# Kernel tuning notes

Measured on AMD Instinct MI355X. Metric: run time of the kernel, lower is better.

## Reference

```python
import jax, jax.numpy as jnp
import numpy as np

B, L, H, N = 4, 4096, 1024, 16
EPS = 1e-6  # layer_norm_epsilon


def setup_inputs() -> dict:
    key = jax.random.key(0)
    ks = jax.random.split(key, 8)
    hidden_states = jax.random.normal(ks[0], (B, L, H), dtype=jnp.float32)
    attention_mask = jnp.ones((B, L), dtype=jnp.float32)
    norm_weight = jnp.ones((H,), dtype=jnp.float32)
    # S4D init: dt log-uniform in [1e-3, 1e-1]; S4D-Lin A init; random C, D
    dt_min, dt_max = 1e-3, 1e-1
    log_dt = jax.random.uniform(ks[1], (H,), dtype=jnp.float32) * (
        float(np.log(dt_max)) - float(np.log(dt_min))) + float(np.log(dt_min))
    log_A_real = jnp.log(0.5 * jnp.ones((H, N), dtype=jnp.float32))
    A_imag = jnp.broadcast_to(float(np.pi) * jnp.arange(N, dtype=jnp.float32), (H, N))
    C_real = jax.random.normal(ks[2], (H, N), dtype=jnp.float32) * (0.5 ** 0.5)
    C_imag = jax.random.normal(ks[3], (H, N), dtype=jnp.float32) * (0.5 ** 0.5)
    D = jax.random.normal(ks[4], (H,), dtype=jnp.float32)
    out_w = jax.random.normal(ks[5], (2 * H, H), dtype=jnp.float32) * 0.02  # 1x1 conv to 2H (GLU)
    out_b = jnp.zeros((2 * H,), dtype=jnp.float32)
    return dict(hidden_states=hidden_states, attention_mask=attention_mask,
                norm_weight=norm_weight, log_dt=log_dt, log_A_real=log_A_real,
                A_imag=A_imag, C_real=C_real, C_imag=C_imag, D=D,
                out_w=out_w, out_b=out_b)


def _s4d_kernel(log_dt, log_A_real, A_imag, C_real, C_imag, length):
    """Diagonal SSM convolution kernel k[h, l] (S4D ZOH discretization)."""
    dt = jnp.exp(log_dt)                                   # (H,)
    A = -jnp.exp(log_A_real) + 1j * A_imag                 # (H, N) complex64
    C = C_real + 1j * C_imag                               # (H, N)
    dtA = A * dt[:, None]                                  # (H, N)
    C_disc = C * (jnp.exp(dtA) - 1.0) / A                  # (H, N)
    vand = jnp.exp(dtA[:, :, None] * jnp.arange(length, dtype=jnp.float32))  # (H, N, L)
    k = 2.0 * jnp.einsum('hn,hnl->hl', C_disc, vand).real  # (H, L)
    return k.astype(jnp.float32)


def reference(hidden_states, attention_mask, norm_weight, log_dt, log_A_real,
              A_imag, C_real, C_imag, D, out_w, out_b):
    # LongT5LayerNorm: RMSNorm (no mean subtraction), variance in fp32
    var = jnp.mean(jnp.square(hidden_states.astype(jnp.float32)), axis=-1, keepdims=True)
    normed = hidden_states * jax.lax.rsqrt(var + EPS) * norm_weight  # (B, L, H)
    # mask padded positions, go to channel-major layout (B, H, L)
    u = (normed * attention_mask[..., None]).transpose(0, 2, 1)
    Lx = u.shape[-1]
    k = _s4d_kernel(log_dt, log_A_real, A_imag, C_real, C_imag, Lx)  # (H, L)
    # causal convolution via FFT of length 2L
    nfft = 2 * Lx
    k_f = jnp.fft.rfft(k, n=nfft)                 # (H, nfft//2+1)
    u_f = jnp.fft.rfft(u, n=nfft)                 # (B, H, nfft//2+1)
    y = jnp.fft.irfft(u_f * k_f, n=nfft)[..., :Lx]  # (B, H, L)
    y = y + u * D[:, None]                        # skip connection
    y = jax.nn.gelu(y, approximate=False)         # torch nn.GELU (exact)
    # output 1x1 conv to 2H, then GLU over the channel dim
    z = jnp.einsum('bhl,oh->bol', y, out_w) + out_b[:, None]
    a, b = jnp.split(z, 2, axis=1)
    ssm_out = (a * jax.nn.sigmoid(b)).transpose(0, 2, 1)  # (B, L, H)
    # residual + dropout (eval mode -> identity)
    return hidden_states + ssm_out
```

## Files before the change

### kernel.cpp

```cpp
#include <hip/hip_runtime.h>

#define B_   4
#define L_   4096
#define H_   1024
#define N_   16
#define CH_  64
#define NC_  (L_/CH_)
#define M_   (B_*L_)
#define O2_  (2*H_)
#define EPS_ 1e-6f

typedef __attribute__((ext_vector_type(4))) float  f32x4;
typedef __attribute__((ext_vector_type(8))) __bf16 bf16x8;

__device__ __forceinline__ unsigned short f2bf(float x) {
  union { float f; unsigned int u; } v; v.f = x;
  unsigned int r = v.u + 0x7FFFu + ((v.u >> 16) & 1u);
  return (unsigned short)(r >> 16);
}
__device__ __forceinline__ float bf2f(unsigned short x) {
  union { unsigned int u; float f; } v; v.u = ((unsigned int)x) << 16;
  return v.f;
}

__device__ __forceinline__ void async_copy16(const void* g, void* l) {
  __builtin_amdgcn_global_load_lds(
      (const __attribute__((address_space(1))) unsigned int*)g,
      (__attribute__((address_space(3))) unsigned int*)l, 16, 0, 0);
}

__global__ void k_prep(const float* __restrict__ log_dt,
                       const float* __restrict__ log_A_real,
                       const float* __restrict__ A_imag,
                       const float* __restrict__ C_real,
                       const float* __restrict__ C_imag,
                       const float* __restrict__ outw,
                       const float* __restrict__ outb,
                       float* __restrict__ wr,  float* __restrict__ wi,
                       float* __restrict__ c2r, float* __restrict__ c2i,
                       float* __restrict__ wpr, float* __restrict__ wpi,
                       unsigned short* __restrict__ Wbf,
                       float* __restrict__ bp) {
  int idx = blockIdx.x * 256 + threadIdx.x;
  int p = idx >> 10, hh = idx & (H_ - 1);
  size_t src = (size_t)((p >> 1) + (p & 1) * H_) * H_ + hh;
  Wbf[idx] = f2bf(outw[src]);
  if (idx < O2_) bp[idx] = outb[(idx >> 1) + (idx & 1) * H_];
  if (idx < H_ * N_) {
    int h = idx / N_, n = idx % N_;
    int hn = h * N_ + n;
    float dt  = expf(log_dt[h]);
    float Ar  = -expf(log_A_real[hn]);
    float Ai  = A_imag[hn];
    float dr  = Ar * dt, di = Ai * dt;
    float er  = expf(dr);
    float wrv = er * cosf(di), wiv = er * sinf(di);
    float e1r = wrv - 1.0f, e1i = wiv;
    float den = Ar * Ar + Ai * Ai;
    float qr  = (e1r * Ar + e1i * Ai) / den;
    float qi  = (e1i * Ar - e1r * Ai) / den;
    float Cr  = C_real[hn], Ci = C_imag[hn];
    float cdr = Cr * qr - Ci * qi;
    float cdi = Cr * qi + Ci * qr;
    float ep  = expf((float)CH_ * dr);
    int o = n * H_ + h;
    wr[o]  = wrv;  wi[o]  = wiv;
    c2r[o] = 2.0f * cdr; c2i[o] = 2.0f * cdi;
    wpr[o] = ep * cosf((float)CH_ * di);
    wpi[o] = ep * sinf((float)CH_ * di);
  }
}

__global__ __launch_bounds__(256) void k_scale(const float* __restrict__ hs,
                                               const float* __restrict__ mask,
                                               float* __restrict__ scale) {
  int m = blockIdx.x, tid = threadIdx.x;
  float4 v = reinterpret_cast<const float4*>(hs + (size_t)m * H_)[tid];
  float s = v.x * v.x + v.y * v.y + v.z * v.z + v.w * v.w;
  #pragma unroll
  for (int off = 32; off > 0; off >>= 1) s += __shfl_down(s, off, 64);
  __shared__ float ps[4];
  if ((tid & 63) == 0) ps[tid >> 6] = s;
  __syncthreads();
  if (tid == 0) {
    float var = (ps[0] + ps[1] + ps[2] + ps[3]) * (1.0f / H_);
    scale[m] = rsqrtf(var + EPS_) * mask[m];
  }
}

__global__ __launch_bounds__(256) void k_scan1(const float* __restrict__ hs,
                                               const float* __restrict__ nw,
                                               const float* __restrict__ scale,
                                               const float* __restrict__ wr_,
                                               const float* __restrict__ wi_,
                                               float* __restrict__ endr,
                                               float* __restrict__ endi,
                                               unsigned short* __restrict__ ubf) {
  int tid = threadIdx.x;
  int h = blockIdx.x * 256 + tid;
  int c = blockIdx.y, b = blockIdx.z;
  float wr[N_], wi[N_], xr[N_], xi[N_];
  #pragma unroll
  for (int n = 0; n < N_; n++) {
    wr[n] = wr_[n * H_ + h]; wi[n] = wi_[n * H_ + h];
    xr[n] = 0.f; xi[n] = 0.f;
  }
  float nwh = nw[h];
  __shared__ float ssc[CH_];
  int l0 = c * CH_;
  if (tid < CH_) ssc[tid] = scale[(size_t)b * L_ + l0 + tid];
  __syncthreads();
  const float* hp = hs + ((size_t)b * L_ + l0) * H_ + h;
  unsigned short* up = ubf + ((size_t)b * L_ + l0) * H_ + h;
  #pragma unroll 8
  for (int l = 0; l < CH_; l++) {
    float u = hp[(size_t)l * H_] * ssc[l] * nwh;
    unsigned short ub = f2bf(u);
    up[(size_t)l * H_] = ub;
    u = bf2f(ub);
    #pragma unroll
    for (int n = 0; n < N_; n++) {
      float oxr = xr[n];
      xr[n] = fmaf(wr[n], oxr, fmaf(-wi[n], xi[n], u));
      xi[n] = fmaf(wr[n], xi[n], wi[n] * oxr);
    }
  }
  size_t base = (((size_t)b * NC_ + c) * N_) * H_ + h;
  #pragma unroll
  for (int n = 0; n < N_; n++) {
    endr[base + (size_t)n * H_] = xr[n];
    endi[base + (size_t)n * H_] = xi[n];
  }
}

__global__ __launch_bounds__(256) void k_carry(const float* __restrict__ wpr_,
                                               const float* __restrict__ wpi_,
                                               const float* __restrict__ endr,
                                               const float* __restrict__ endi,
                                               float* __restrict__ carr,
                                               float* __restrict__ cari) {
  int idx = blockIdx.x * 256 + threadIdx.x;
  int h = idx & (H_ - 1);
  int n = (idx >> 10) & (N_ - 1);
  int b = idx >> 14;
  float wprv = wpr_[n * H_ + h], wpiv = wpi_[n * H_ + h];
  float sr = 0.f, si = 0.f;
  size_t cstride = (size_t)N_ * H_;
  size_t base = ((size_t)b * NC_) * cstride + (size_t)n * H_ + h;
  for (int c = 0; c < NC_; c++, base += cstride) {
    carr[base] = sr; cari[base] = si;
    float er = endr[base], ei = endi[base];
    float osr = sr;
    sr = fmaf(wprv, osr,  fmaf(-wpiv, si, er));
    si = fmaf(wprv, si, fmaf(wpiv, osr, ei));
  }
}

__global__ __launch_bounds__(256) void k_scan2(const unsigned short* __restrict__ ubf,
                                               const float* __restrict__ wr_,
                                               const float* __restrict__ wi_,
                                               const float* __restrict__ c2r_,
                                               const float* __restrict__ c2i_,
                                               const float* __restrict__ Dp,
                                               const float* __restrict__ carr,
                                               const float* __restrict__ cari,
                                               unsigned short* __restrict__ ybf) {
  int tid = threadIdx.x;
  int h = blockIdx.x * 256 + tid;
  int c = blockIdx.y, b = blockIdx.z;
  float wr[N_], wi[N_], cr[N_], ci[N_], xr[N_], xi[N_];
  size_t base = (((size_t)b * NC_ + c) * N_) * H_ + h;
  #pragma unroll
  for (int n = 0; n < N_; n++) {
    wr[n] = wr_[n * H_ + h]; wi[n] = wi_[n * H_ + h];
    cr[n] = c2r_[n * H_ + h]; ci[n] = c2i_[n * H_ + h];
    xr[n] = carr[base + (size_t)n * H_];
    xi[n] = cari[base + (size_t)n * H_];
  }
  float Dh = Dp[h];
  int l0 = c * CH_;
  const unsigned short* up = ubf + ((size_t)b * L_ + l0) * H_ + h;
  unsigned short* yp = ybf + ((size_t)b * L_ + l0) * H_ + h;
  #pragma unroll 8
  for (int l = 0; l < CH_; l++) {
    float u = bf2f(up[(size_t)l * H_]);
    float yv = u * Dh;
    #pragma unroll
    for (int n = 0; n < N_; n++) {
      float oxr = xr[n];
      xr[n] = fmaf(wr[n], oxr, fmaf(-wi[n], xi[n], u));
      xi[n] = fmaf(wr[n], xi[n], wi[n] * oxr);
      yv = fmaf(cr[n], xr[n], yv);
      yv = fmaf(-ci[n], xi[n], yv);
    }
    float g = 0.5f * yv * (1.0f + erff(yv * 0.70710678118654752f));
    yp[(size_t)l * H_] = f2bf(g);
  }
}

#define BM 128
#define BN 128
#define BK 32
#define GSTRIDE 68
__global__ __launch_bounds__(256) void k_gemm(const unsigned short* __restrict__ A,
                                              const unsigned short* __restrict__ Bw,
                                              const float* __restrict__ bp,
                                              const float* __restrict__ hs,
                                              float* __restrict__ out) {
  __shared__ __align__(16) char smem[BM * GSTRIDE * 4];
  unsigned short* As = (unsigned short*)smem;
  unsigned short* Bs = As + BM * BK;
  float* gt = (float*)smem;
  const int tid  = threadIdx.x;
  const int lane = tid & 63;
  const int wave = tid >> 6;
  const int bn = blockIdx.x * BN;
  const int bm = blockIdx.y * BM;
  const int wm = (wave >> 1) * 64;
  const int wn = (wave & 1) * 64;
  const int K = H_;
  f32x4 acc[4][4];
  #pragma unroll
  for (int mi = 0; mi < 4; mi++)
    #pragma unroll
    for (int ni = 0; ni < 4; ni++) acc[mi][ni] = (f32x4){0.f, 0.f, 0.f, 0.f};

  const int g0 = tid, g1 = 256 + tid;
  const int r0 = g0 >> 2, c0 = ((g0 & 3) ^ ((r0 >> 1) & 3)) * 8;
  const int r1 = g1 >> 2, c1 = ((g1 & 3) ^ ((r1 >> 1) & 3)) * 8;
  const int ar = lane & 15, kqi = lane >> 4;

  for (int k0 = 0; k0 < K; k0 += BK) {
    async_copy16(A  + (size_t)(bm + r0) * K + k0 + c0, &As[g0 * 8]);
    async_copy16(A  + (size_t)(bm + r1) * K + k0 + c1, &As[g1 * 8]);
    async_copy16(Bw + (size_t)(bn + r0) * K + k0 + c0, &Bs[g0 * 8]);
    async_copy16(Bw + (size_t)(bn + r1) * K + k0 + c1, &Bs[g1 * 8]);
    __syncthreads();
    bf16x8 af[4], bf[4];
    #pragma unroll
    for (int mi = 0; mi < 4; mi++) {
      int row = wm + mi * 16 + ar;
      af[mi] = *reinterpret_cast<const bf16x8*>(&As[row * BK + ((kqi ^ ((row >> 1) & 3)) * 8)]);
    }
    #pragma unroll
    for (int ni = 0; ni < 4; ni++) {
      int row = wn + ni * 16 + ar;
      bf[ni] = *reinterpret_cast<const bf16x8*>(&Bs[row * BK + ((kqi ^ ((row >> 1) & 3)) * 8)]);
    }
    #pragma unroll
    for (int mi = 0; mi < 4; mi++)
      #pragma unroll
      for (int ni = 0; ni < 4; ni++)
        acc[mi][ni] = __builtin_amdgcn_mfma_f32_16x16x32_bf16(af[mi], bf[ni], acc[mi][ni], 0, 0, 0);
    __syncthreads();
  }
  #pragma unroll
  for (int ni = 0; ni < 4; ni++) {
    int p  = wn + ni * 16 + (lane & 15);
    int pe = (bn + p) & ~1;
    float bA = bp[pe], bB = bp[pe + 1];
    int jl = p >> 1;
    #pragma unroll
    for (int mi = 0; mi < 4; mi++) {
      int row0 = wm + mi * 16 + (lane >> 4) * 4;
      #pragma unroll
      for (int r = 0; r < 4; r++) {
        float v = acc[mi][ni][r];
        float w = __shfl_xor(v, 1, 64);
        if (!(lane & 1))
          gt[(row0 + r) * GSTRIDE + jl] = (v + bA) / (1.0f + __expf(-(w + bB)));
      }
    }
  }
  __syncthreads();
  {
    int c4 = tid & 15;
    int rr = tid >> 4;
    size_t obase = (size_t)bm * H_ + (bn >> 1);
    #pragma unroll
    for (int rep = 0; rep < 8; rep++) {
      int row = rep * 16 + rr;
      float4 g = *reinterpret_cast<const float4*>(&gt[row * GSTRIDE + c4 * 4]);
      size_t o = obase + (size_t)row * H_ + c4 * 4;
      float4 hv = *reinterpret_cast<const float4*>(&hs[o]);
      float4 rv = {hv.x + g.x, hv.y + g.y, hv.z + g.z, hv.w + g.w};
      *reinterpret_cast<float4*>(&out[o]) = rv;
    }
  }
}

extern "C" void kernel_launch(void* const* d_in, const int* in_sizes, int n_in,
                              void* d_out, int out_size, void* d_ws, size_t ws_size,
                              hipStream_t stream) {
  const float* hs    = (const float*)d_in[0];
  const float* mask  = (const float*)d_in[1];
  const float* nw    = (const float*)d_in[2];
  const float* ldt   = (const float*)d_in[3];
  const float* lar   = (const float*)d_in[4];
  const float* aim   = (const float*)d_in[5];
  const float* crl   = (const float*)d_in[6];
  const float* cim   = (const float*)d_in[7];
  const float* Dp    = (const float*)d_in[8];
  const float* outw  = (const float*)d_in[9];
  const float* outb  = (const float*)d_in[10];
  float* out = (float*)d_out;

  size_t off = 0;
  char* ws = (char*)d_ws;
  auto nxt = [&](size_t bytes) -> void* {
    void* p = ws + off; off += (bytes + 255) & ~(size_t)255; return p;
  };
  float* wr   = (float*)nxt(H_ * N_ * 4);
  float* wi   = (float*)nxt(H_ * N_ * 4);
  float* c2r  = (float*)nxt(H_ * N_ * 4);
  float* c2i  = (float*)nxt(H_ * N_ * 4);
  float* wpr  = (float*)nxt(H_ * N_ * 4);
  float* wpi  = (float*)nxt(H_ * N_ * 4);
  float* bpck = (float*)nxt(O2_ * 4);
  float* scale= (float*)nxt((size_t)M_ * 4);
  float* endr = (float*)nxt((size_t)B_ * NC_ * N_ * H_ * 4);
  float* endi = (float*)nxt((size_t)B_ * NC_ * N_ * H_ * 4);
  float* carr = (float*)nxt((size_t)B_ * NC_ * N_ * H_ * 4);
  float* cari = (float*)nxt((size_t)B_ * NC_ * N_ * H_ * 4);
  unsigned short* Wbf = (unsigned short*)nxt((size_t)O2_ * H_ * 2);
  unsigned short* ubf = (unsigned short*)nxt((size_t)M_ * H_ * 2);
  unsigned short* ybf = (unsigned short*)nxt((size_t)M_ * H_ * 2);

  k_prep<<<dim3(O2_ * H_ / 256), dim3(256), 0, stream>>>(ldt, lar, aim, crl, cim,
                                                         outw, outb,
                                                         wr, wi, c2r, c2i, wpr, wpi,
                                                         Wbf, bpck);
  k_scale<<<dim3(M_), dim3(256), 0, stream>>>(hs, mask, scale);
  k_scan1<<<dim3(H_ / 256, NC_, B_), dim3(256), 0, stream>>>(hs, nw, scale, wr, wi,
                                                             endr, endi, ubf);
  k_carry<<<dim3(B_ * N_ * H_ / 256), dim3(256), 0, stream>>>(wpr, wpi, endr, endi, carr, cari);
  k_scan2<<<dim3(H_ / 256, NC_, B_), dim3(256), 0, stream>>>(ubf, wr, wi, c2r, c2i,
                                                             Dp, carr, cari, ybf);
  k_gemm<<<dim3(O2_ / BN, M_ / BM), dim3(256), 0, stream>>>(ybf, Wbf, bpck, hs, out);
}
```

Baseline: 366.9 us.

## Double GEMM K-tile to 64 with new swizzle, prefetch residual, drop scan smem

The GEMM K-step grows from 32 to 64, so each iteration loads twice as much A/B data with one barrier pair. The LDS XOR swizzle is rewritten for 8 chunks per row, and the MFMA loop is split into two k-halves. The residual hidden_states tile is now loaded into registers before the epilogue so its global latency overlaps the GLU computation. The scan kernel also drops its shared-memory staging of the per-row scale and its barrier, reading the scale directly from global memory instead. The trade-off is higher register pressure and double the LDS tile size, which fits within the existing 34 KB buffer.

```diff
diff --git a/kernel.cpp b/kernel.cpp
--- a/kernel.cpp
+++ b/kernel.cpp
@@ -106,15 +106,13 @@
     xr[n] = 0.f; xi[n] = 0.f;
   }
   float nwh = nw[h];
-  __shared__ float ssc[CH_];
   int l0 = c * CH_;
-  if (tid < CH_) ssc[tid] = scale[(size_t)b * L_ + l0 + tid];
-  __syncthreads();
+  const float* scp = scale + (size_t)b * L_ + l0;
   const float* hp = hs + ((size_t)b * L_ + l0) * H_ + h;
   unsigned short* up = ubf + ((size_t)b * L_ + l0) * H_ + h;
   #pragma unroll 8
   for (int l = 0; l < CH_; l++) {
-    float u = hp[(size_t)l * H_] * ssc[l] * nwh;
+    float u = hp[(size_t)l * H_] * scp[l] * nwh;
     unsigned short ub = f2bf(u);
     up[(size_t)l * H_] = ub;
     u = bf2f(ub);
@@ -200,7 +198,7 @@
 
 #define BM 128
 #define BN 128
-#define BK 32
+#define BKG 64
 #define GSTRIDE 68
 __global__ __launch_bounds__(256) void k_gemm(const unsigned short* __restrict__ A,
                                               const unsigned short* __restrict__ Bw,
@@ -209,7 +207,7 @@
                                               float* __restrict__ out) {
   __shared__ __align__(16) char smem[BM * GSTRIDE * 4];
   unsigned short* As = (unsigned short*)smem;
-  unsigned short* Bs = As + BM * BK;
+  unsigned short* Bs = As + BM * BKG;
   float* gt = (float*)smem;
   const int tid  = threadIdx.x;
   const int lane = tid & 63;
@@ -225,34 +223,55 @@
     #pragma unroll
     for (int ni = 0; ni < 4; ni++) acc[mi][ni] = (f32x4){0.f, 0.f, 0.f, 0.f};
 
-  const int g0 = tid, g1 = 256 + tid;
-  const int r0 = g0 >> 2, c0 = ((g0 & 3) ^ ((r0 >> 1) & 3)) * 8;
-  const int r1 = g1 >> 2, c1 = ((g1 & 3) ^ ((r1 >> 1) & 3)) * 8;
+  int rr[4], cc[4];
+  #pragma unroll
+  for (int i = 0; i < 4; i++) {
+    int g = i * 256 + tid;
+    rr[i] = g >> 3;
+    cc[i] = ((g & 7) ^ (rr[i] & 7)) * 8;
+  }
   const int ar = lane & 15, kqi = lane >> 4;
 
-  for (int k0 = 0; k0 < K; k0 += BK) {
-    async_copy16(A  + (size_t)(bm + r0) * K + k0 + c0, &As[g0 * 8]);
-    async_copy16(A  + (size_t)(bm + r1) * K + k0 + c1, &As[g1 * 8]);
-    async_copy16(Bw + (size_t)(bn + r0) * K + k0 + c0, &Bs[g0 * 8]);
-    async_copy16(Bw + (size_t)(bn + r1) * K + k0 + c1, &Bs[g1 * 8]);
+  for (int k0 = 0; k0 < K; k0 += BKG) {
+    #pragma unroll
+    for (int i = 0; i < 4; i++)
+      async_copy16(A + (size_t)(bm + rr[i]) * K + k0 + cc[i], &As[(i * 256 + tid) * 8]);
+    #pragma unroll
+    for (int i = 0; i < 4; i++)
+      async_copy16(Bw + (size_t)(bn + rr[i]) * K + k0 + cc[i], &Bs[(i * 256 + tid) * 8]);
     __syncthreads();
-    bf16x8 af[4], bf[4];
-    #pragma unroll
-    for (int mi = 0; mi < 4; mi++) {
-      int row = wm + mi * 16 + ar;
-      af[mi] = *reinterpret_cast<const bf16x8*>(&As[row * BK + ((kqi ^ ((row >> 1) & 3)) * 8)]);
+    #pragma unroll
+    for (int kh = 0; kh < 2; kh++) {
+      bf16x8 af[4], bf[4];
+      #pragma unroll
+      for (int mi = 0; mi < 4; mi++) {
+        int row = wm + mi * 16 + ar;
+        af[mi] = *reinterpret_cast<const bf16x8*>(
+            &As[row * BKG + (((kh * 4 + kqi) ^ (row & 7)) * 8)]);
+      }
+      #pragma unroll
+      for (int ni = 0; ni < 4; ni++) {
+        int row = wn + ni * 16 + ar;
+        bf[ni] = *reinterpret_cast<const bf16x8*>(
+            &Bs[row * BKG + (((kh * 4 + kqi) ^ (row & 7)) * 8)]);
+      }
+      #pragma unroll
+      for (int mi = 0; mi < 4; mi++)
+        #pragma unroll
+        for (int ni = 0; ni < 4; ni++)
+          acc[mi][ni] = __builtin_amdgcn_mfma_f32_16x16x32_bf16(af[mi], bf[ni], acc[mi][ni], 0, 0, 0);
     }
-    #pragma unroll
-    for (int ni = 0; ni < 4; ni++) {
-      int row = wn + ni * 16 + ar;
-      bf[ni] = *reinterpret_cast<const bf16x8*>(&Bs[row * BK + ((kqi ^ ((row >> 1) & 3)) * 8)]);
-    }
-    #pragma unroll
-    for (int mi = 0; mi < 4; mi++)
-      #pragma unroll
-      for (int ni = 0; ni < 4; ni++)
-        acc[mi][ni] = __builtin_amdgcn_mfma_f32_16x16x32_bf16(af[mi], bf[ni], acc[mi][ni], 0, 0, 0);
     __syncthreads();
+  }
+
+  const int c4 = tid & 15;
+  const int rw = tid >> 4;
+  const size_t obase = (size_t)bm * H_ + (bn >> 1);
+  float4 hv[8];
+  #pragma unroll
+  for (int rep = 0; rep < 8; rep++) {
+    int row = rep * 16 + rw;
+    hv[rep] = *reinterpret_cast<const float4*>(&hs[obase + (size_t)row * H_ + c4 * 4]);
   }
   #pragma unroll
   for (int ni = 0; ni < 4; ni++) {
@@ -273,19 +292,13 @@
     }
   }
   __syncthreads();
-  {
-    int c4 = tid & 15;
-    int rr = tid >> 4;
-    size_t obase = (size_t)bm * H_ + (bn >> 1);
-    #pragma unroll
-    for (int rep = 0; rep < 8; rep++) {
-      int row = rep * 16 + rr;
-      float4 g = *reinterpret_cast<const float4*>(&gt[row * GSTRIDE + c4 * 4]);
-      size_t o = obase + (size_t)row * H_ + c4 * 4;
-      float4 hv = *reinterpret_cast<const float4*>(&hs[o]);
-      float4 rv = {hv.x + g.x, hv.y + g.y, hv.z + g.z, hv.w + g.w};
-      *reinterpret_cast<float4*>(&out[o]) = rv;
-    }
+  #pragma unroll
+  for (int rep = 0; rep < 8; rep++) {
+    int row = rep * 16 + rw;
+    float4 g = *reinterpret_cast<const float4*>(&gt[row * GSTRIDE + c4 * 4]);
+    size_t o = obase + (size_t)row * H_ + c4 * 4;
+    float4 rv = {hv[rep].x + g.x, hv[rep].y + g.y, hv[rep].z + g.z, hv[rep].w + g.w};
+    *reinterpret_cast<float4*>(&out[o]) = rv;
   }
 }
 
```

Result: no change. 363.1 us (-1.0%).
